# Optimization experiments

Hardware: AMD Instinct MI355X
Metric: run time of the kernel (lower is better)

## Reference

```python
import jax, jax.numpy as jnp
import numpy as np

B, IN, OUT = 2048, 64, 2048


def setup_inputs() -> dict:
    key = jax.random.key(0)
    k1, k2, k3 = jax.random.split(key, 3)
    x = jax.random.normal(k1, (B, IN), dtype=jnp.float32)
    # learned params (shapes per init: means [in, out], inv_std_dev [out, in, in])
    means = jax.random.uniform(k2, (IN, OUT), dtype=jnp.float32)
    # roughly like the inverse of a diagonal step matrix plus small noise
    inv_std_dev = (jax.random.normal(k3, (OUT, IN, IN), dtype=jnp.float32) * 0.05
                   + jnp.eye(IN, dtype=jnp.float32) * 0.5)
    return {"x": x, "means": means, "inv_std_dev": inv_std_dev}


def reference(x, means, inv_std_dev):
    # diff[b, o, i] = x[b, i] - means[i, o]   -> [B, OUT, IN]
    d = x[:, None, :] - means.T[None, :, :]
    # torch uses inv_std_dev.pow(2) (elementwise square), not a matrix square
    A = inv_std_dev * inv_std_dev  # [OUT, IN, IN]
    # per-neuron quadratic form: q[b, o] = d[b,o,:] @ A[o] @ d[b,o,:]
    q = jnp.einsum('boi,oij,boj->bo', d, A, d)
    return jnp.exp(-0.5 * q)  # [B, OUT]
```

## Files before the change

### kernel.cpp

```cpp
#include <hip/hip_runtime.h>
#include <hip/hip_bf16.h>

typedef __bf16 bf16x8 __attribute__((ext_vector_type(8)));
typedef float f32x16 __attribute__((ext_vector_type(16)));

#define B_N 2048
#define O_N 2048
#define K_TRI 2080
#define K_TOT 2304
#define K_STEPS 36
#define ROWB (K_TOT * 2)

__device__ __forceinline__ void gld16(const void* g, void* l) {
    __builtin_amdgcn_global_load_lds(
        (const __attribute__((address_space(1))) void*)g,
        (__attribute__((address_space(3))) void*)l,
        16, 0, 0);
}

__global__ __launch_bounds__(256) void rbf_prep2(
    const float* __restrict__ inv, const float* __restrict__ means,
    const float* __restrict__ x, __bf16* __restrict__ S, __bf16* __restrict__ P)
{
    __shared__ float s[64 * 65];
    __shared__ float mld[64];
    __shared__ float uw[128];
    __shared__ unsigned short ptab[K_TRI];

    const int t = threadIdx.x;
    {
        int base = 0;
#pragma unroll 1
        for (int i = 0; i < 64; ++i) {
            if (t < 64 - i) ptab[base + t] = (unsigned short)((i << 8) | (i + t));
            base += 64 - i;
        }
    }

    if ((int)blockIdx.x < O_N) {
        const int o = blockIdx.x;
        const float4* src = (const float4*)(inv + (size_t)o * 4096);
#pragma unroll
        for (int k = 0; k < 4; ++k) {
            const int idx = k * 256 + t;
            const float4 v = src[idx];
            const int i = idx >> 4;
            const int j0 = (idx & 15) * 4;
            s[i * 65 + j0 + 0] = v.x * v.x;
            s[i * 65 + j0 + 1] = v.y * v.y;
            s[i * 65 + j0 + 2] = v.z * v.z;
            s[i * 65 + j0 + 3] = v.w * v.w;
        }
        if (t < 64) mld[t] = means[(size_t)t * O_N + o];
        __syncthreads();
        if (t < 64) {
            float u = 0.f;
#pragma unroll
            for (int i = 0; i < 64; ++i) u = fmaf(s[i * 65 + t], mld[i], u);
            uw[t] = u;
        } else if (t < 128) {
            const int j = t - 64;
            float w = 0.f;
#pragma unroll
            for (int i = 0; i < 64; ++i) w = fmaf(s[j * 65 + i], mld[i], w);
            uw[64 + j] = w;
        }
        __syncthreads();
        __bf16* Srow = S + (size_t)o * K_TOT;
#pragma unroll 1
        for (int p = t; p < K_TRI; p += 256) {
            const int ij = ptab[p];
            const int i = ij >> 8, j = ij & 255;
            const float v = (i == j) ? s[i * 65 + i]
                                     : (s[i * 65 + j] + s[j * 65 + i]);
            Srow[p] = (__bf16)v;
        }
        if (t < 64) {
            const float c = -(uw[t] + uw[64 + t]);
            const __bf16 hi = (__bf16)c;
            const __bf16 lo = (__bf16)(c - (float)hi);
            Srow[K_TRI + t] = hi;
            Srow[K_TRI + 64 + t] = hi;
            Srow[K_TRI + 128 + t] = lo;
        }
        if (t == 0) {
            float kk = 0.f;
#pragma unroll
            for (int j = 0; j < 64; ++j) kk = fmaf(uw[j], mld[j], kk);
            const __bf16 khi = (__bf16)kk;
            const __bf16 klo = (__bf16)(kk - (float)khi);
            Srow[2272] = khi;
            Srow[2273] = klo;
        }
        if (t < K_TOT - 2274) Srow[2274 + t] = (__bf16)0.f;
    } else {
        const int b = (int)blockIdx.x - O_N;
        if (t < 64) mld[t] = x[(size_t)b * 64 + t];
        __syncthreads();
        __bf16* Prow = P + (size_t)b * K_TOT;
#pragma unroll 1
        for (int p = t; p < K_TRI; p += 256) {
            const int ij = ptab[p];
            Prow[p] = (__bf16)(mld[ij >> 8] * mld[ij & 255]);
        }
        if (t < 64) {
            const float v = mld[t];
            const __bf16 hi = (__bf16)v;
            Prow[K_TRI + t] = hi;
            Prow[K_TRI + 64 + t] = (__bf16)(v - (float)hi);
            Prow[K_TRI + 128 + t] = hi;
        }
        if (t == 0) {
            Prow[2272] = (__bf16)1.f;
            Prow[2273] = (__bf16)1.f;
        }
        if (t < K_TOT - 2274) Prow[2274 + t] = (__bf16)0.f;
    }
}

__global__ __launch_bounds__(256, 1) void rbf_gemm(
    const __bf16* __restrict__ P, const __bf16* __restrict__ S,
    float* __restrict__ out)
{
    __shared__ __align__(16) char sAB[4][32768];

    const int tid = threadIdx.x;
    const int lane = tid & 63;
    const int w = tid >> 6;
    const int wr = w >> 1, wc = w & 1;
    const int cl = lane & 31;
    const int h = lane >> 5;

    const int wg = (int)blockIdx.x;
    const int xcd = wg & 7;
    const int loc = wg >> 3;
    const int oBase = (xcd * 2 + (loc & 1)) * 128;
    const int bBase = (loc >> 1) * 128;

    const char* gsrc[8];
    int ldst[8];
#pragma unroll
    for (int r = 0; r < 8; ++r) {
        const int Ld = r * 4096 + tid * 16;
        ldst[r] = Ld;
        const int Lo = Ld & 16383;
        const int ks = Lo >> 11;
        const int row = (Lo >> 4) & 127;
        gsrc[r] = ((Ld >> 14) ? (const char*)S + (size_t)(oBase + row) * ROWB
                              : (const char*)P + (size_t)(bBase + row) * ROWB)
                  + ks * 16;
    }

#define RBF_STAGE(ST) do {                                                    \
    const size_t go_ = (size_t)(ST) * 128;                                    \
    char* d_ = &sAB[(ST) & 3][0];                                             \
    _Pragma("unroll")                                                         \
    for (int r_ = 0; r_ < 8; ++r_)                                            \
        gld16(gsrc[r_] + go_, d_ + ldst[r_]);                                 \
} while (0)

    RBF_STAGE(0);
    RBF_STAGE(1);

    const f32x16 zz = {0.f,0.f,0.f,0.f,0.f,0.f,0.f,0.f,
                       0.f,0.f,0.f,0.f,0.f,0.f,0.f,0.f};
    f32x16 acc00 = zz, acc01 = zz, acc10 = zz, acc11 = zz;

    const int aoff = (wr * 64 + cl) * 16;
    const int boff = 16384 + (wc * 64 + cl) * 16;

#pragma unroll 1
    for (int st = 0; st < K_STEPS; ++st) {
        if (st + 2 < K_STEPS) {
            RBF_STAGE(st + 2);
            asm volatile("s_waitcnt vmcnt(16)" ::: "memory");
        } else if (st + 1 < K_STEPS) {
            asm volatile("s_waitcnt vmcnt(8)" ::: "memory");
        } else {
            asm volatile("s_waitcnt vmcnt(0)" ::: "memory");
        }
        __builtin_amdgcn_s_barrier();
        const char* bp = &sAB[st & 3][0];

        __builtin_amdgcn_s_setprio(1);
#pragma unroll
        for (int sl = 0; sl < 4; ++sl) {
            const int kso = (sl * 2 + h) * 2048;
            const bf16x8 a0 = *(const bf16x8*)(bp + kso + aoff);
            const bf16x8 a1 = *(const bf16x8*)(bp + kso + aoff + 512);
            const bf16x8 b0 = *(const bf16x8*)(bp + kso + boff);
            const bf16x8 b1 = *(const bf16x8*)(bp + kso + boff + 512);
            acc00 = __builtin_amdgcn_mfma_f32_32x32x16_bf16(a0, b0, acc00, 0, 0, 0);
            acc01 = __builtin_amdgcn_mfma_f32_32x32x16_bf16(a0, b1, acc01, 0, 0, 0);
            acc10 = __builtin_amdgcn_mfma_f32_32x32x16_bf16(a1, b0, acc10, 0, 0, 0);
            acc11 = __builtin_amdgcn_mfma_f32_32x32x16_bf16(a1, b1, acc11, 0, 0, 0);
        }
        __builtin_amdgcn_s_setprio(0);
    }
#undef RBF_STAGE

#pragma unroll
    for (int r = 0; r < 16; ++r) {
        const int row32 = (r & 3) + 8 * (r >> 2) + 4 * h;
        const size_t r0 = (size_t)(bBase + wr * 64 + row32) * O_N;
        const size_t r1 = (size_t)(bBase + wr * 64 + 32 + row32) * O_N;
        const int c0 = oBase + wc * 64 + cl;
        const int c1 = oBase + wc * 64 + 32 + cl;
        out[r0 + c0] = exp2f(acc00[r] * -0.72134752044448170368f);
        out[r0 + c1] = exp2f(acc01[r] * -0.72134752044448170368f);
        out[r1 + c0] = exp2f(acc10[r] * -0.72134752044448170368f);
        out[r1 + c1] = exp2f(acc11[r] * -0.72134752044448170368f);
    }
}

extern "C" void kernel_launch(void* const* d_in, const int* in_sizes, int n_in,
                              void* d_out, int out_size, void* d_ws, size_t ws_size,
                              hipStream_t stream)
{
    const float* x = (const float*)d_in[0];
    const float* means = (const float*)d_in[1];
    const float* inv = (const float*)d_in[2];
    float* out = (float*)d_out;

    __bf16* S = (__bf16*)d_ws;
    __bf16* P = (__bf16*)((char*)d_ws + (size_t)O_N * K_TOT * sizeof(__bf16));

    rbf_prep2<<<dim3(2 * O_N), dim3(256), 0, stream>>>(inv, means, x, S, P);
    rbf_gemm<<<dim3(256), dim3(256), 0, stream>>>(P, S, out);

    (void)in_sizes; (void)n_in; (void)out_size; (void)ws_size;
}
```

Baseline: 69.09 us.

## Store GEMM operands in chunk-major layout and batch prep rows per block

The prep kernel now writes S and P in a chunk-major tiled layout, where each 16-byte k-chunk of 2048 rows is contiguous. Each block processes 8 rows and stages them in shared memory so it can emit coalesced 16-byte stores instead of scattered per-element bf16 writes. The GEMM's global-to-LDS loads now read fully contiguous 2 KB segments per k-chunk rather than row-strided 16-byte pieces. The cost is a grid shrunk from 4096 to 512 prep blocks, each doing serial per-row work, which may reduce parallelism in the prep stage.

```diff
diff --git a/kernel.cpp b/kernel.cpp
--- a/kernel.cpp
+++ b/kernel.cpp
@@ -9,7 +9,7 @@
 #define K_TRI 2080
 #define K_TOT 2304
 #define K_STEPS 36
-#define ROWB (K_TOT * 2)
+#define CHUNKS 288
 
 __device__ __forceinline__ void gld16(const void* g, void* l) {
     __builtin_amdgcn_global_load_lds(
@@ -18,14 +18,15 @@
         16, 0, 0);
 }
 
-__global__ __launch_bounds__(256) void rbf_prep2(
+__global__ __launch_bounds__(256) void rbf_prep3(
     const float* __restrict__ inv, const float* __restrict__ means,
-    const float* __restrict__ x, __bf16* __restrict__ S, __bf16* __restrict__ P)
+    const float* __restrict__ x, __bf16* __restrict__ St, __bf16* __restrict__ Pt)
 {
     __shared__ float s[64 * 65];
     __shared__ float mld[64];
     __shared__ float uw[128];
     __shared__ unsigned short ptab[K_TRI];
+    __shared__ unsigned short obuf[CHUNKS * 64];
 
     const int t = threadIdx.x;
     {
@@ -36,85 +37,99 @@
             base += 64 - i;
         }
     }
-
-    if ((int)blockIdx.x < O_N) {
-        const int o = blockIdx.x;
-        const float4* src = (const float4*)(inv + (size_t)o * 4096);
-#pragma unroll
-        for (int k = 0; k < 4; ++k) {
-            const int idx = k * 256 + t;
-            const float4 v = src[idx];
-            const int i = idx >> 4;
-            const int j0 = (idx & 15) * 4;
-            s[i * 65 + j0 + 0] = v.x * v.x;
-            s[i * 65 + j0 + 1] = v.y * v.y;
-            s[i * 65 + j0 + 2] = v.z * v.z;
-            s[i * 65 + j0 + 3] = v.w * v.w;
-        }
-        if (t < 64) mld[t] = means[(size_t)t * O_N + o];
+    const bool isS = (int)blockIdx.x < 256;
+    const int g0 = (isS ? (int)blockIdx.x : (int)blockIdx.x - 256) * 8;
+
+    if (isS) {
+#pragma unroll 1
+        for (int r8 = 0; r8 < 8; ++r8) {
+            const int o = g0 + r8;
+            __syncthreads();
+            const float4* src = (const float4*)(inv + (size_t)o * 4096);
+#pragma unroll
+            for (int k = 0; k < 4; ++k) {
+                const int idx = k * 256 + t;
+                const float4 v = src[idx];
+                const int i = idx >> 4;
+                const int j0 = (idx & 15) * 4;
+                s[i * 65 + j0 + 0] = v.x * v.x;
+                s[i * 65 + j0 + 1] = v.y * v.y;
+                s[i * 65 + j0 + 2] = v.z * v.z;
+                s[i * 65 + j0 + 3] = v.w * v.w;
+            }
+            if (t < 64) mld[t] = means[(size_t)t * O_N + o];
+            __syncthreads();
+            if (t < 64) {
+                float u = 0.f;
+#pragma unroll
+                for (int i = 0; i < 64; ++i) u = fmaf(s[i * 65 + t], mld[i], u);
+                uw[t] = u;
+            } else if (t < 128) {
+                const int j = t - 64;
+                float w = 0.f;
+#pragma unroll
+                for (int i = 0; i < 64; ++i) w = fmaf(s[j * 65 + i], mld[i], w);
+                uw[64 + j] = w;
+            }
+            __syncthreads();
+#pragma unroll 1
+            for (int c = t; c < K_TOT; c += 256) {
+                float v;
+                if (c < K_TRI) {
+                    const int ij = ptab[c];
+                    const int i = ij >> 8, j = ij & 255;
+                    v = (i == j) ? s[i * 65 + i] : (s[i * 65 + j] + s[j * 65 + i]);
+                } else if (c < 2272) {
+                    const int j = (c - K_TRI) & 63;
+                    const float cv = -(uw[j] + uw[64 + j]);
+                    const __bf16 hi = (__bf16)cv;
+                    v = (c < 2208) ? (float)hi : (cv - (float)hi);
+                } else if (c < 2274) {
+                    float kk = 0.f;
+#pragma unroll
+                    for (int j = 0; j < 64; ++j) kk = fmaf(uw[j], mld[j], kk);
+                    const __bf16 khi = (__bf16)kk;
+                    v = (c == 2272) ? (float)khi : (kk - (float)khi);
+                } else v = 0.f;
+                obuf[(c >> 3) * 64 + r8 * 8 + (c & 7)] =
+                    __builtin_bit_cast(unsigned short, (__bf16)v);
+            }
+        }
+    } else {
+#pragma unroll
+        for (int q = 0; q < 2; ++q) {
+            const int idx = q * 256 + t;
+            s[(idx >> 6) * 65 + (idx & 63)] = x[(size_t)(g0 + (idx >> 6)) * 64 + (idx & 63)];
+        }
         __syncthreads();
-        if (t < 64) {
-            float u = 0.f;
-#pragma unroll
-            for (int i = 0; i < 64; ++i) u = fmaf(s[i * 65 + t], mld[i], u);
-            uw[t] = u;
-        } else if (t < 128) {
-            const int j = t - 64;
-            float w = 0.f;
-#pragma unroll
-            for (int i = 0; i < 64; ++i) w = fmaf(s[j * 65 + i], mld[i], w);
-            uw[64 + j] = w;
-        }
-        __syncthreads();
-        __bf16* Srow = S + (size_t)o * K_TOT;
-#pragma unroll 1
-        for (int p = t; p < K_TRI; p += 256) {
-            const int ij = ptab[p];
-            const int i = ij >> 8, j = ij & 255;
-            const float v = (i == j) ? s[i * 65 + i]
-                                     : (s[i * 65 + j] + s[j * 65 + i]);
-            Srow[p] = (__bf16)v;
-        }
-        if (t < 64) {
-            const float c = -(uw[t] + uw[64 + t]);
-            const __bf16 hi = (__bf16)c;
-            const __bf16 lo = (__bf16)(c - (float)hi);
-            Srow[K_TRI + t] = hi;
-            Srow[K_TRI + 64 + t] = hi;
-            Srow[K_TRI + 128 + t] = lo;
-        }
-        if (t == 0) {
-            float kk = 0.f;
-#pragma unroll
-            for (int j = 0; j < 64; ++j) kk = fmaf(uw[j], mld[j], kk);
-            const __bf16 khi = (__bf16)kk;
-            const __bf16 klo = (__bf16)(kk - (float)khi);
-            Srow[2272] = khi;
-            Srow[2273] = klo;
-        }
-        if (t < K_TOT - 2274) Srow[2274 + t] = (__bf16)0.f;
-    } else {
-        const int b = (int)blockIdx.x - O_N;
-        if (t < 64) mld[t] = x[(size_t)b * 64 + t];
-        __syncthreads();
-        __bf16* Prow = P + (size_t)b * K_TOT;
-#pragma unroll 1
-        for (int p = t; p < K_TRI; p += 256) {
-            const int ij = ptab[p];
-            Prow[p] = (__bf16)(mld[ij >> 8] * mld[ij & 255]);
-        }
-        if (t < 64) {
-            const float v = mld[t];
-            const __bf16 hi = (__bf16)v;
-            Prow[K_TRI + t] = hi;
-            Prow[K_TRI + 64 + t] = (__bf16)(v - (float)hi);
-            Prow[K_TRI + 128 + t] = hi;
-        }
-        if (t == 0) {
-            Prow[2272] = (__bf16)1.f;
-            Prow[2273] = (__bf16)1.f;
-        }
-        if (t < K_TOT - 2274) Prow[2274 + t] = (__bf16)0.f;
+#pragma unroll 1
+        for (int r8 = 0; r8 < 8; ++r8) {
+            const float* xr = &s[r8 * 65];
+#pragma unroll 1
+            for (int c = t; c < K_TOT; c += 256) {
+                float v;
+                if (c < K_TRI) {
+                    const int ij = ptab[c];
+                    v = xr[ij >> 8] * xr[ij & 255];
+                } else if (c < 2272) {
+                    const float xv = xr[(c - K_TRI) & 63];
+                    const __bf16 hi = (__bf16)xv;
+                    v = (c < 2144) ? (float)hi
+                      : (c < 2208) ? (xv - (float)hi) : (float)hi;
+                } else if (c < 2274) v = 1.f;
+                else v = 0.f;
+                obuf[(c >> 3) * 64 + r8 * 8 + (c & 7)] =
+                    __builtin_bit_cast(unsigned short, (__bf16)v);
+            }
+        }
+    }
+    __syncthreads();
+    __bf16* dst = isS ? St : Pt;
+#pragma unroll 1
+    for (int idx = t; idx < CHUNKS * 8; idx += 256) {
+        const int chunk = idx >> 3, r8 = idx & 7;
+        const bf16x8 v = *(const bf16x8*)&obuf[chunk * 64 + r8 * 8];
+        *(bf16x8*)(dst + ((size_t)chunk * 2048 + g0 + r8) * 8) = v;
     }
 }
 
@@ -138,25 +153,21 @@
     const int bBase = (loc >> 1) * 128;
 
     const char* gsrc[8];
-    int ldst[8];
 #pragma unroll
     for (int r = 0; r < 8; ++r) {
-        const int Ld = r * 4096 + tid * 16;
-        ldst[r] = Ld;
-        const int Lo = Ld & 16383;
-        const int ks = Lo >> 11;
-        const int row = (Lo >> 4) & 127;
-        gsrc[r] = ((Ld >> 14) ? (const char*)S + (size_t)(oBase + row) * ROWB
-                              : (const char*)P + (size_t)(bBase + row) * ROWB)
-                  + ks * 16;
+        const int ks = (r & 3) * 2 + (tid >> 7);
+        const int row = tid & 127;
+        gsrc[r] = (r < 4)
+            ? (const char*)P + ((size_t)ks * 2048 + bBase + row) * 16
+            : (const char*)S + ((size_t)ks * 2048 + oBase + row) * 16;
     }
 
 #define RBF_STAGE(ST) do {                                                    \
-    const size_t go_ = (size_t)(ST) * 128;                                    \
+    const size_t go_ = (size_t)(ST) * 262144;      \
     char* d_ = &sAB[(ST) & 3][0];                                             \
     _Pragma("unroll")                                                         \
     for (int r_ = 0; r_ < 8; ++r_)                                            \
-        gld16(gsrc[r_] + go_, d_ + ldst[r_]);                                 \
+        gld16(gsrc[r_] + go_, d_ + r_ * 4096 + tid * 16);                     \
 } while (0)
 
     RBF_STAGE(0);
@@ -222,11 +233,11 @@
     const float* inv = (const float*)d_in[2];
     float* out = (float*)d_out;
 
-    __bf16* S = (__bf16*)d_ws;
-    __bf16* P = (__bf16*)((char*)d_ws + (size_t)O_N * K_TOT * sizeof(__bf16));
-
-    rbf_prep2<<<dim3(2 * O_N), dim3(256), 0, stream>>>(inv, means, x, S, P);
-    rbf_gemm<<<dim3(256), dim3(256), 0, stream>>>(P, S, out);
+    __bf16* St = (__bf16*)d_ws;
+    __bf16* Pt = (__bf16*)((char*)d_ws + (size_t)K_STEPS * 8 * 2048 * 16);
+
+    rbf_prep3<<<dim3(512), dim3(256), 0, stream>>>(inv, means, x, St, Pt);
+    rbf_gemm<<<dim3(256), dim3(256), 0, stream>>>(Pt, St, out);
 
     (void)in_sizes; (void)n_in; (void)out_size; (void)ws_size;
 }
```

Result: faster. 63.51 us (-8.1%).
